# Kernel tuning notes

Hardware: AMD Instinct MI355X
Metric: run time of the kernel (lower is better)

## Reference

```python
import jax, jax.numpy as jnp
from jax import lax
import numpy as np

BINS = 256

def setup_inputs() -> dict:
    key = jax.random.key(0)
    k1, k2 = jax.random.split(key)
    B, C, H, W = 8, 3, 1024, 1024
    dst = jax.random.uniform(k1, (B, C, H, W), dtype=jnp.float32)
    ref = jax.random.uniform(k2, (B, C, H, W), dtype=jnp.float32)
    return {"dst": dst, "ref": ref}


def _cal_hist(img):
    # img: [B,C,H,W] in [0,1]. torch.histc(img*255, bins=256, min=0, max=255):
    # bin width = 255/256, so bin = floor(img*255 / (255/256)) = floor(img*256).
    # Inputs are in [0,1) so nothing is out of histc's range (clip is a no-op safeguard).
    B, C, H, W = img.shape
    bc = B * C
    x = img.reshape(bc, H * W)
    idx = jnp.clip(jnp.floor(x * float(BINS)).astype(jnp.int32), 0, BINS - 1)
    rows = jnp.arange(bc, dtype=jnp.int32)[:, None]
    counts = jnp.zeros((bc, BINS), jnp.float32).at[rows, idx].add(1.0)
    # F.normalize(p=1, dim=1) with eps=1e-12
    counts = counts / jnp.maximum(jnp.sum(counts, axis=1, keepdims=True), 1e-12)
    # triu-bmm == cumulative sum -> per-channel CDF
    return jnp.cumsum(counts, axis=1)


def _trans_row(cdf_dst, cdf_ref):
    # Faithful vectorization of the sequential two-pointer loop in cal_trans.
    # For each i (pointer j only ever advances): match at the smallest
    # j' >= j with cdf_ref[j'-1] <= d <= cdf_ref[j']; if impossible, j runs
    # off to 256 and this and all later entries become 255.
    def step(j, d):
        s = jnp.searchsorted(cdf_ref, d)            # smallest s with cdf_ref[s] >= d, in [0,256]
        cand = jnp.maximum(j, s)                    # pointer never moves backwards; cand in [1,256]
        ok = (j < BINS) & (cand <= BINS - 1) & (d >= cdf_ref[cand - 1])
        out = jnp.where(ok, cand, BINS - 1)
        j_next = jnp.where(ok, cand, jnp.int32(BINS))
        return j_next, out.astype(jnp.int32)
    _, tail = lax.scan(step, jnp.int32(1), cdf_dst[1:])  # i = 1..255
    table = jnp.concatenate([jnp.zeros(1, jnp.int32), tail])  # table[0] = arange init = 0
    return table.at[BINS - 1].set(BINS - 1)                   # table[:,255] = 255


def reference(dst, ref):
    B, C, H, W = dst.shape
    bc = B * C
    hist_dst = _cal_hist(dst)   # [BC,256] CDFs
    hist_ref = _cal_hist(ref)
    tables = jax.vmap(_trans_row)(hist_dst, hist_ref)  # [BC,256] int32
    # NOTE: original code indexes tables[b*c] (not b*C+c) -- bug preserved faithfully.
    b_idx = jnp.arange(B, dtype=jnp.int32)[:, None]
    c_idx = jnp.arange(C, dtype=jnp.int32)[None, :]
    row_sel = (b_idx * c_idx).reshape(-1)               # [BC]
    luts = tables[row_sel]                              # [BC,256]
    pix = jnp.clip((dst * 255.0).astype(jnp.int32), 0, BINS - 1).reshape(bc, H * W)
    rst = jnp.take_along_axis(luts, pix, axis=1).reshape(B, C, H, W)
    return rst.astype(dst.dtype) / 255.0
```

## Files before the change

kernel.cpp:

```cpp
#include <hip/hip_runtime.h>

#define BINS 256
#define BC_N 24
#define C_N  3
#define NROWS 12
#define CH   32
#define ACH  128

__global__ __launch_bounds__(512) void hm_hist(const float* __restrict__ dst,
                                               const float* __restrict__ refp,
                                               unsigned int* __restrict__ part,
                                               int n4_per_row) {
    __shared__ unsigned int shist[BINS];
    __shared__ unsigned int wsum[3][BINS];

    const int t = threadIdx.x;
    const int l = t & 63;
    const int w = t >> 6;

    if (t < BINS) shist[t] = 0u;
    __syncthreads();

    const int y = blockIdx.y;
    const int row = (y < 9) ? y : 2 * y - 8;
    const float* img = blockIdx.z ? refp : dst;
    const int span = n4_per_row / CH;
    const float4* p = reinterpret_cast<const float4*>(img)
                    + (size_t)row * n4_per_row + (size_t)blockIdx.x * span;

    const int nsl = span >> 6;
    const int na  = (nsl * 75) >> 7;

    if (w < 5) {
        const int per = na / 5;
        const int rem = na - per * 5;
        int s   = w * per + min(w, rem);
        int cnt = per + (w < rem ? 1 : 0);
        for (; cnt >= 3; cnt -= 3, s += 3) {
            float4 v0 = p[((s + 0) << 6) + l];
            float4 v1 = p[((s + 1) << 6) + l];
            float4 v2 = p[((s + 2) << 6) + l];
            __builtin_amdgcn_sched_barrier(0);
            atomicAdd(&shist[min((int)(v0.x * 256.0f), 255)], 1u);
            atomicAdd(&shist[min((int)(v0.y * 256.0f), 255)], 1u);
            atomicAdd(&shist[min((int)(v0.z * 256.0f), 255)], 1u);
            atomicAdd(&shist[min((int)(v0.w * 256.0f), 255)], 1u);
            atomicAdd(&shist[min((int)(v1.x * 256.0f), 255)], 1u);
            atomicAdd(&shist[min((int)(v1.y * 256.0f), 255)], 1u);
            atomicAdd(&shist[min((int)(v1.z * 256.0f), 255)], 1u);
            atomicAdd(&shist[min((int)(v1.w * 256.0f), 255)], 1u);
            atomicAdd(&shist[min((int)(v2.x * 256.0f), 255)], 1u);
            atomicAdd(&shist[min((int)(v2.y * 256.0f), 255)], 1u);
            atomicAdd(&shist[min((int)(v2.z * 256.0f), 255)], 1u);
            atomicAdd(&shist[min((int)(v2.w * 256.0f), 255)], 1u);
        }
        for (; cnt > 0; --cnt, ++s) {
            float4 v = p[(s << 6) + l];
            atomicAdd(&shist[min((int)(v.x * 256.0f), 255)], 1u);
            atomicAdd(&shist[min((int)(v.y * 256.0f), 255)], 1u);
            atomicAdd(&shist[min((int)(v.z * 256.0f), 255)], 1u);
            atomicAdd(&shist[min((int)(v.w * 256.0f), 255)], 1u);
        }
        if (w == 0) {
            for (int j = (nsl << 6) + l; j < span; j += 64) {
                float4 v = p[j];
                atomicAdd(&shist[min((int)(v.x * 256.0f), 255)], 1u);
                atomicAdd(&shist[min((int)(v.y * 256.0f), 255)], 1u);
                atomicAdd(&shist[min((int)(v.z * 256.0f), 255)], 1u);
                atomicAdd(&shist[min((int)(v.w * 256.0f), 255)], 1u);
            }
            if (blockIdx.x == CH - 1) {
                const float4* pr = reinterpret_cast<const float4*>(img)
                                 + (size_t)row * n4_per_row;
                for (int j = CH * span + l; j < n4_per_row; j += 64) {
                    float4 v = pr[j];
                    atomicAdd(&shist[min((int)(v.x * 256.0f), 255)], 1u);
                    atomicAdd(&shist[min((int)(v.y * 256.0f), 255)], 1u);
                    atomicAdd(&shist[min((int)(v.z * 256.0f), 255)], 1u);
                    atomicAdd(&shist[min((int)(v.w * 256.0f), 255)], 1u);
                }
            }
        }
    } else {
        const unsigned long long t0 = (l & 1)  ? 0ull : ~0ull;
        const unsigned long long t1 = (l & 2)  ? 0ull : ~0ull;
        const unsigned long long t2 = (l & 4)  ? 0ull : ~0ull;
        const unsigned long long t3 = (l & 8)  ? 0ull : ~0ull;
        const unsigned long long t4 = (l & 16) ? 0ull : ~0ull;
        const unsigned long long t5 = (l & 32) ? 0ull : ~0ull;
        unsigned int c0 = 0, c1 = 0, c2 = 0, c3 = 0;

        auto grp = [&](float x) {
            int bin = min((int)(x * 256.0f), 255);
            unsigned long long B0 = __ballot(bin & 1);
            unsigned long long B1 = __ballot(bin & 2);
            unsigned long long B2 = __ballot(bin & 4);
            unsigned long long B3 = __ballot(bin & 8);
            unsigned long long B4 = __ballot(bin & 16);
            unsigned long long B5 = __ballot(bin & 32);
            unsigned long long B6 = __ballot(bin & 64);
            unsigned long long B7 = __ballot(bin & 128);
            unsigned long long m = (B0 ^ t0) & (B1 ^ t1) & (B2 ^ t2)
                                 & (B3 ^ t3) & (B4 ^ t4) & (B5 ^ t5);
            unsigned long long a = m & ~B7, b = m & B7;
            c0 += (unsigned)__popcll(a & ~B6);
            c1 += (unsigned)__popcll(a &  B6);
            c2 += (unsigned)__popcll(b & ~B6);
            c3 += (unsigned)__popcll(b &  B6);
        };

        int s = na + (w - 5);
        if (s < nsl) {
            float4 v = p[(s << 6) + l];
            for (; s + 3 < nsl; s += 3) {
                float4 nv = p[((s + 3) << 6) + l];
                __builtin_amdgcn_sched_barrier(0);
                grp(v.x); grp(v.y); grp(v.z); grp(v.w);
                v = nv;
            }
            grp(v.x); grp(v.y); grp(v.z); grp(v.w);
        }
        wsum[w - 5][l]       = c0;
        wsum[w - 5][l + 64]  = c1;
        wsum[w - 5][l + 128] = c2;
        wsum[w - 5][l + 192] = c3;
    }
    __syncthreads();

    if (t < BINS) {
        unsigned int sv = shist[t] + wsum[0][t] + wsum[1][t] + wsum[2][t];
        part[(((size_t)blockIdx.z * NROWS + y) * CH + blockIdx.x) * BINS + t] = sv;
    }
}

__global__ __launch_bounds__(256) void hm_table(const unsigned int* __restrict__ part,
                                                float* __restrict__ lut) {
    __shared__ unsigned int sd[BINS], sr[BINS];
    __shared__ float cdf_d[BINS], cdf_r[BINS];
    __shared__ int firstFail;

    const int r = blockIdx.x;
    const int t = threadIdx.x;

    const unsigned int* pd = part + ((size_t)0 * NROWS + r) * CH * BINS;
    const unsigned int* pr = part + ((size_t)1 * NROWS + r) * CH * BINS;
    unsigned int xd = 0, xr = 0;
    #pragma unroll 8
    for (int k = 0; k < CH; ++k) {
        xd += pd[k * BINS + t];
        xr += pr[k * BINS + t];
    }
    if (t == 0) firstFail = BINS;
    sd[t] = xd; sr[t] = xr;
    __syncthreads();

    #pragma unroll
    for (int off = 1; off < BINS; off <<= 1) {
        unsigned int yd = (t >= off) ? sd[t - off] : 0u;
        unsigned int yr = (t >= off) ? sr[t - off] : 0u;
        __syncthreads();
        xd += yd; xr += yr;
        sd[t] = xd; sr[t] = xr;
        __syncthreads();
    }
    float totd = fmaxf((float)sd[BINS - 1], 1e-12f);
    float totr = fmaxf((float)sr[BINS - 1], 1e-12f);
    cdf_d[t] = (float)xd / totd;
    cdf_r[t] = (float)xr / totr;
    __syncthreads();

    int out;
    if (t == 0) {
        out = 0;
    } else {
        float d = cdf_d[t];
        int lo = 0, hi = BINS;
        while (lo < hi) {
            int m = (lo + hi) >> 1;
            if (cdf_r[m] < d) lo = m + 1; else hi = m;
        }
        int cand = lo > 1 ? lo : 1;
        bool ok = (cand <= BINS - 1) && (d >= cdf_r[cand - 1]);
        if (!ok) atomicMin(&firstFail, t);
        out = cand;
    }
    __syncthreads();

    if (t >= firstFail) out = BINS - 1;
    if (t == BINS - 1) out = BINS - 1;
    lut[(size_t)r * BINS + t] = (float)out / 255.0f;
}

__global__ __launch_bounds__(256) void hm_apply(const float* __restrict__ dst,
                                                const float* __restrict__ lut,
                                                float* __restrict__ out,
                                                int n4_per_row) {
    __shared__ float slut[BINS];
    const int bc = blockIdx.y;
    const int b = bc / C_N;
    const int c = bc - b * C_N;
    const int r = b * c;
    const int cr = (r <= 8) ? r : 8 + ((r - 8) >> 1);
    const int t = threadIdx.x;

    slut[t] = lut[(size_t)cr * BINS + t];
    __syncthreads();

    const float4* in4 = reinterpret_cast<const float4*>(dst) + (size_t)bc * n4_per_row;
    float4* out4 = reinterpret_cast<float4*>(out) + (size_t)bc * n4_per_row;
    const int gsz = gridDim.x * 256;

    int i = blockIdx.x * 256 + t;
    for (; i + gsz < n4_per_row; i += 2 * gsz) {
        float4 v0 = in4[i];
        float4 v1 = in4[i + gsz];
        __builtin_amdgcn_sched_barrier(0);
        float4 o0, o1;
        o0.x = slut[min(max((int)(v0.x * 255.0f), 0), 255)];
        o0.y = slut[min(max((int)(v0.y * 255.0f), 0), 255)];
        o0.z = slut[min(max((int)(v0.z * 255.0f), 0), 255)];
        o0.w = slut[min(max((int)(v0.w * 255.0f), 0), 255)];
        o1.x = slut[min(max((int)(v1.x * 255.0f), 0), 255)];
        o1.y = slut[min(max((int)(v1.y * 255.0f), 0), 255)];
        o1.z = slut[min(max((int)(v1.z * 255.0f), 0), 255)];
        o1.w = slut[min(max((int)(v1.w * 255.0f), 0), 255)];
        out4[i] = o0;
        out4[i + gsz] = o1;
    }
    for (; i < n4_per_row; i += gsz) {
        float4 v = in4[i];
        float4 o;
        o.x = slut[min(max((int)(v.x * 255.0f), 0), 255)];
        o.y = slut[min(max((int)(v.y * 255.0f), 0), 255)];
        o.z = slut[min(max((int)(v.z * 255.0f), 0), 255)];
        o.w = slut[min(max((int)(v.w * 255.0f), 0), 255)];
        out4[i] = o;
    }
}

extern "C" void kernel_launch(void* const* d_in, const int* in_sizes, int n_in,
                              void* d_out, int out_size, void* d_ws, size_t ws_size,
                              hipStream_t stream) {
    const float* dst  = (const float*)d_in[0];
    const float* refp = (const float*)d_in[1];
    float* out = (float*)d_out;

    const int total = in_sizes[0];
    const int hw = total / BC_N;
    const int n4 = hw >> 2;

    unsigned int* part = (unsigned int*)d_ws;
    float* lut = (float*)((char*)d_ws + (size_t)2 * NROWS * CH * BINS * sizeof(unsigned int));

    dim3 hg(CH, NROWS, 2);
    hm_hist<<<hg, dim3(512), 0, stream>>>(dst, refp, part, n4);

    hm_table<<<dim3(NROWS), dim3(256), 0, stream>>>(part, lut);

    dim3 ag(ACH, BC_N);
    hm_apply<<<ag, dim3(256), 0, stream>>>(dst, lut, out, n4);
}
```

Baseline: 70.05 us.

## Use smaller 256-thread histogram blocks with more chunks per row

The histogram kernel now runs 256-thread blocks: three waves do LDS atomics and one wave does ballot-based counting. Each row is split into 85 chunks instead of 32, so there are more blocks, and the work ratio between the atomic and ballot paths is retuned to about 19%. The tail handling is folded into a simple strided loop. This is meant to improve occupancy and load balance across CUs, at the cost of more partial histograms for the table kernel to reduce.

```diff
diff --git a/kernel.cpp b/kernel.cpp
--- a/kernel.cpp
+++ b/kernel.cpp
@@ -4,82 +4,42 @@
 #define BC_N 24
 #define C_N  3
 #define NROWS 12
-#define CH   32
+#define CH   85
 #define ACH  128
 
-__global__ __launch_bounds__(512) void hm_hist(const float* __restrict__ dst,
+__global__ __launch_bounds__(256) void hm_hist(const float* __restrict__ dst,
                                                const float* __restrict__ refp,
                                                unsigned int* __restrict__ part,
                                                int n4_per_row) {
     __shared__ unsigned int shist[BINS];
-    __shared__ unsigned int wsum[3][BINS];
+    __shared__ unsigned int wsum[BINS];
 
     const int t = threadIdx.x;
     const int l = t & 63;
     const int w = t >> 6;
 
-    if (t < BINS) shist[t] = 0u;
+    shist[t] = 0u;
     __syncthreads();
 
     const int y = blockIdx.y;
     const int row = (y < 9) ? y : 2 * y - 8;
     const float* img = blockIdx.z ? refp : dst;
-    const int span = n4_per_row / CH;
-    const float4* p = reinterpret_cast<const float4*>(img)
-                    + (size_t)row * n4_per_row + (size_t)blockIdx.x * span;
-
-    const int nsl = span >> 6;
-    const int na  = (nsl * 75) >> 7;
-
-    if (w < 5) {
-        const int per = na / 5;
-        const int rem = na - per * 5;
-        int s   = w * per + min(w, rem);
-        int cnt = per + (w < rem ? 1 : 0);
-        for (; cnt >= 3; cnt -= 3, s += 3) {
-            float4 v0 = p[((s + 0) << 6) + l];
-            float4 v1 = p[((s + 1) << 6) + l];
-            float4 v2 = p[((s + 2) << 6) + l];
-            __builtin_amdgcn_sched_barrier(0);
-            atomicAdd(&shist[min((int)(v0.x * 256.0f), 255)], 1u);
-            atomicAdd(&shist[min((int)(v0.y * 256.0f), 255)], 1u);
-            atomicAdd(&shist[min((int)(v0.z * 256.0f), 255)], 1u);
-            atomicAdd(&shist[min((int)(v0.w * 256.0f), 255)], 1u);
-            atomicAdd(&shist[min((int)(v1.x * 256.0f), 255)], 1u);
-            atomicAdd(&shist[min((int)(v1.y * 256.0f), 255)], 1u);
-            atomicAdd(&shist[min((int)(v1.z * 256.0f), 255)], 1u);
-            atomicAdd(&shist[min((int)(v1.w * 256.0f), 255)], 1u);
-            atomicAdd(&shist[min((int)(v2.x * 256.0f), 255)], 1u);
-            atomicAdd(&shist[min((int)(v2.y * 256.0f), 255)], 1u);
-            atomicAdd(&shist[min((int)(v2.z * 256.0f), 255)], 1u);
-            atomicAdd(&shist[min((int)(v2.w * 256.0f), 255)], 1u);
-        }
-        for (; cnt > 0; --cnt, ++s) {
-            float4 v = p[(s << 6) + l];
+    const float4* p = reinterpret_cast<const float4*>(img) + (size_t)row * n4_per_row;
+
+    const int span = (n4_per_row + CH - 1) / CH;
+    const int lo = blockIdx.x * span;
+    const int hi = min(lo + span, n4_per_row);
+    const int n  = hi - lo;
+    const int SB = ((n * 19) / 100) & ~63;
+    const int mid = hi - SB;
+
+    if (w < 3) {
+        for (int i = lo + w * 64 + l; i < mid; i += 192) {
+            float4 v = p[i];
             atomicAdd(&shist[min((int)(v.x * 256.0f), 255)], 1u);
             atomicAdd(&shist[min((int)(v.y * 256.0f), 255)], 1u);
             atomicAdd(&shist[min((int)(v.z * 256.0f), 255)], 1u);
             atomicAdd(&shist[min((int)(v.w * 256.0f), 255)], 1u);
-        }
-        if (w == 0) {
-            for (int j = (nsl << 6) + l; j < span; j += 64) {
-                float4 v = p[j];
-                atomicAdd(&shist[min((int)(v.x * 256.0f), 255)], 1u);
-                atomicAdd(&shist[min((int)(v.y * 256.0f), 255)], 1u);
-                atomicAdd(&shist[min((int)(v.z * 256.0f), 255)], 1u);
-                atomicAdd(&shist[min((int)(v.w * 256.0f), 255)], 1u);
-            }
-            if (blockIdx.x == CH - 1) {
-                const float4* pr = reinterpret_cast<const float4*>(img)
-                                 + (size_t)row * n4_per_row;
-                for (int j = CH * span + l; j < n4_per_row; j += 64) {
-                    float4 v = pr[j];
-                    atomicAdd(&shist[min((int)(v.x * 256.0f), 255)], 1u);
-                    atomicAdd(&shist[min((int)(v.y * 256.0f), 255)], 1u);
-                    atomicAdd(&shist[min((int)(v.z * 256.0f), 255)], 1u);
-                    atomicAdd(&shist[min((int)(v.w * 256.0f), 255)], 1u);
-                }
-            }
         }
     } else {
         const unsigned long long t0 = (l & 1)  ? 0ull : ~0ull;
@@ -109,28 +69,26 @@
             c3 += (unsigned)__popcll(b &  B6);
         };
 
-        int s = na + (w - 5);
-        if (s < nsl) {
-            float4 v = p[(s << 6) + l];
-            for (; s + 3 < nsl; s += 3) {
-                float4 nv = p[((s + 3) << 6) + l];
+        const int nk = SB >> 6;
+        if (nk > 0) {
+            float4 v = p[mid + l];
+            for (int k = 0; k + 1 < nk; ++k) {
+                float4 nv = p[mid + ((k + 1) << 6) + l];
                 __builtin_amdgcn_sched_barrier(0);
                 grp(v.x); grp(v.y); grp(v.z); grp(v.w);
                 v = nv;
             }
             grp(v.x); grp(v.y); grp(v.z); grp(v.w);
         }
-        wsum[w - 5][l]       = c0;
-        wsum[w - 5][l + 64]  = c1;
-        wsum[w - 5][l + 128] = c2;
-        wsum[w - 5][l + 192] = c3;
-    }
-    __syncthreads();
-
-    if (t < BINS) {
-        unsigned int sv = shist[t] + wsum[0][t] + wsum[1][t] + wsum[2][t];
-        part[(((size_t)blockIdx.z * NROWS + y) * CH + blockIdx.x) * BINS + t] = sv;
-    }
+        wsum[l]       = c0;
+        wsum[l + 64]  = c1;
+        wsum[l + 128] = c2;
+        wsum[l + 192] = c3;
+    }
+    __syncthreads();
+
+    part[(((size_t)blockIdx.z * NROWS + y) * CH + blockIdx.x) * BINS + t]
+        = shist[t] + wsum[t];
 }
 
 __global__ __launch_bounds__(256) void hm_table(const unsigned int* __restrict__ part,
@@ -145,7 +103,7 @@
     const unsigned int* pd = part + ((size_t)0 * NROWS + r) * CH * BINS;
     const unsigned int* pr = part + ((size_t)1 * NROWS + r) * CH * BINS;
     unsigned int xd = 0, xr = 0;
-    #pragma unroll 8
+    #pragma unroll 5
     for (int k = 0; k < CH; ++k) {
         xd += pd[k * BINS + t];
         xr += pr[k * BINS + t];
@@ -253,7 +211,7 @@
     float* lut = (float*)((char*)d_ws + (size_t)2 * NROWS * CH * BINS * sizeof(unsigned int));
 
     dim3 hg(CH, NROWS, 2);
-    hm_hist<<<hg, dim3(512), 0, stream>>>(dst, refp, part, n4);
+    hm_hist<<<hg, dim3(256), 0, stream>>>(dst, refp, part, n4);
 
     hm_table<<<dim3(NROWS), dim3(256), 0, stream>>>(part, lut);
 
```

After: 66.81 us (median of 2 runs). -4.6%, faster.
